# Kernel tuning notes

Measured on AMD Instinct MI355X. Metric: run time of the kernel, lower is better.

## Reference

```python
import jax, jax.numpy as jnp
import numpy as np

MARGIN = 0.3  # init kwarg, mode='norm'


def _pairwise_dist(X):
    # squared euclidean distances, then safe sqrt (matches euc_dist(X.t()).sqrt())
    sq = jnp.sum(X * X, axis=1)                      # [n]
    d2 = sq[:, None] + sq[None, :] - 2.0 * (X @ X.T)  # [n, n]
    d2 = jnp.maximum(d2, 0.0)
    # safe sqrt: avoid inf derivative at 0 (diagonal); forward value identical
    return jnp.where(d2 > 0.0, jnp.sqrt(jnp.where(d2 > 0.0, d2, 1.0)), 0.0)


def setup_inputs() -> dict:
    key = jax.random.key(0)
    kx, ky = jax.random.split(key)
    X = jax.random.normal(kx, (4096, 2048), dtype=jnp.float32)
    Y = jax.random.randint(ky, (4096,), 0, 128, dtype=jnp.int64)
    return {"X": X, "Y": Y}


def reference(X, Y):
    dist = _pairwise_dist(X)                         # [n, n]
    mask = Y[:, None] == Y[None, :]                  # same-identity mask [n, n]
    inf = jnp.array(jnp.inf, dtype=dist.dtype)
    # hardest positive per anchor: max over same-label entries
    dist_ap = jnp.max(jnp.where(mask, dist, -inf), axis=1)  # [n]
    # hardest negative per anchor: min over different-label entries
    dist_an = jnp.min(jnp.where(mask, inf, dist), axis=1)   # [n]
    # mode == 'norm': mean hinge
    return jnp.mean(jnp.maximum(dist_ap - dist_an + MARGIN, 0.0))
```

## Files before the change

### kernel.cpp

```cpp
#include <hip/hip_runtime.h>
#include <hip/hip_bf16.h>
#include <hip/hip_fp8.h>

typedef __attribute__((ext_vector_type(4))) int i32x4;
typedef __attribute__((ext_vector_type(8))) int i32x8;
typedef __attribute__((ext_vector_type(16))) float f32x16;

#define MARGIN 0.3f
#define BIGF 3.0e38f

__device__ __forceinline__ f32x16 mx_mfma(i32x8 a, i32x8 b, f32x16 c) {
    return __builtin_amdgcn_mfma_scale_f32_32x32x64_f8f6f4(
        a, b, c, 0 , 0 ,
        0, 127 , 0, 127 );
}

__device__ __forceinline__ i32x8 ld32(const unsigned char* p) {
    i32x4 lo = *(const i32x4*)p;
    i32x4 hi = *(const i32x4*)(p + 16);
    return __builtin_shufflevector(lo, hi, 0, 1, 2, 3, 4, 5, 6, 7);
}

__global__ __launch_bounds__(256) void convert_norm_kernel(
    const float* __restrict__ X, unsigned char* __restrict__ Xf,
    float* __restrict__ nrm, unsigned* __restrict__ ap,
    unsigned* __restrict__ an, unsigned* __restrict__ cnt, int K) {
    const int wave = threadIdx.x >> 6, lane = threadIdx.x & 63;
    const int row = blockIdx.x * 4 + wave;
    const float* xr = X + (size_t)row * K;
    const size_t pbase = ((size_t)(row >> 5)) << 16;
    const int rsub = row & 31;
    float s = 0.0f;
    for (int c = lane * 8; c < K; c += 64 * 8) {
        float4 v0 = *(const float4*)(xr + c);
        float4 v1 = *(const float4*)(xr + c + 4);
        float f[8] = {v0.x, v0.y, v0.z, v0.w, v1.x, v1.y, v1.z, v1.w};
        union { unsigned char b[8]; uint2 u; } p;
#pragma unroll
        for (int i = 0; i < 8; i++) {
            __hip_fp8_e4m3 q(f[i]);
            p.b[i] = q.__x;
            float d = (float)q;
            s += d * d;
        }
        const int lslot = rsub + (((c >> 5) & 1) << 5);
        unsigned char* dst = Xf + pbase + ((size_t)(c >> 6) << 11)
                             + (lslot << 5) + (c & 31);
        *(uint2*)dst = p.u;
    }
    for (int off = 32; off > 0; off >>= 1) s += __shfl_xor(s, off, 64);
    if (lane == 0) {
        nrm[row] = s;
        ap[row] = 0u;
        an[row] = 0x7F800000u;
        if (row == 0) *cnt = 0u;
    }
}

__global__ __launch_bounds__(256, 4) void gemm_reduce_kernel(
    const unsigned char* __restrict__ Xf, const float* __restrict__ nrm,
    const int* __restrict__ Y, unsigned* __restrict__ ap,
    unsigned* __restrict__ an, unsigned* __restrict__ cnt,
    float* __restrict__ out, int N, int K) {
    __shared__ int sYr[128], sYc[128];
    __shared__ float sNr[128], sNc[128];
    __shared__ float redmax[4][64], redmin[4][64];
    __shared__ float cmax[4][64], cmin[4][64];
    __shared__ float lsum[4];
    __shared__ unsigned s_done;

    const int tid = threadIdx.x;
    const int wave = tid >> 6;
    const int lane = tid & 63;
    const int m = lane & 31;
    const int h = lane >> 5;
    const int wr = wave >> 1;
    const int wc = wave & 1;

    const int NB = N >> 7;
    int bi = blockIdx.x, ti = 0;
    while (bi >= NB - ti) { bi -= NB - ti; ti++; }
    const int tj = ti + bi;
    const int rowBase = ti << 7;
    const int colBase = tj << 7;

    if (tid < 128) {
        sYr[tid] = Y[rowBase + tid];
        sNr[tid] = nrm[rowBase + tid];
    } else {
        const int t0 = tid - 128;
        sYc[t0] = Y[colBase + t0];
        sNc[t0] = nrm[colBase + t0];
    }

    f32x16 acc[2][2];
#pragma unroll
    for (int si = 0; si < 2; si++)
#pragma unroll
        for (int sj = 0; sj < 2; sj++)
#pragma unroll
            for (int rr = 0; rr < 16; rr++) acc[si][sj][rr] = 0.0f;

    const unsigned char* pa[2];
    const unsigned char* pb[2];
#pragma unroll
    for (int si = 0; si < 2; si++)
        pa[si] = Xf + (((size_t)(rowBase >> 5) + wr * 2 + si) << 16) + lane * 32;
#pragma unroll
    for (int sj = 0; sj < 2; sj++)
        pb[sj] = Xf + (((size_t)(colBase >> 5) + wc * 2 + sj) << 16) + lane * 32;

    const int nt = K >> 6;
#pragma unroll 4
    for (int t = 0; t < nt; t++) {
        const size_t off = (size_t)t << 11;
        i32x8 a0 = ld32(pa[0] + off);
        i32x8 a1 = ld32(pa[1] + off);
        i32x8 b0 = ld32(pb[0] + off);
        i32x8 b1 = ld32(pb[1] + off);
        acc[0][0] = mx_mfma(a0, b0, acc[0][0]);
        acc[0][1] = mx_mfma(a0, b1, acc[0][1]);
        acc[1][0] = mx_mfma(a1, b0, acc[1][0]);
        acc[1][1] = mx_mfma(a1, b1, acc[1][1]);
    }

    __syncthreads();

    float cdp[2] = {-1.0f, -1.0f};
    float cdn[2] = {BIGF, BIGF};
#pragma unroll
    for (int si = 0; si < 2; si++)
#pragma unroll
        for (int reg = 0; reg < 16; reg++) {
            const int row64 = si * 32 + (reg & 3) + 8 * (reg >> 2) + 4 * h;
            const int rIdx = wr * 64 + row64;
            const int yr = sYr[rIdx];
            const float nr = sNr[rIdx];
            float dp = -1.0f, dn = BIGF;
#pragma unroll
            for (int sj = 0; sj < 2; sj++) {
                const int cIdx = wc * 64 + sj * 32 + m;
                float d2 = nr + sNc[cIdx] - 2.0f * acc[si][sj][reg];
                float d = sqrtf(fmaxf(d2, 0.0f));
                bool same = (yr == sYc[cIdx]);
                float vp = same ? d : -1.0f;
                float vn = same ? BIGF : d;
                dp = fmaxf(dp, vp);
                dn = fminf(dn, vn);
                cdp[sj] = fmaxf(cdp[sj], vp);
                cdn[sj] = fminf(cdn[sj], vn);
            }
            for (int off = 1; off < 32; off <<= 1) {
                dp = fmaxf(dp, __shfl_xor(dp, off, 64));
                dn = fminf(dn, __shfl_xor(dn, off, 64));
            }
            if (m == 0) {
                redmax[wave][row64] = dp;
                redmin[wave][row64] = dn;
            }
        }
#pragma unroll
    for (int sj = 0; sj < 2; sj++) {
        cdp[sj] = fmaxf(cdp[sj], __shfl_xor(cdp[sj], 32, 64));
        cdn[sj] = fminf(cdn[sj], __shfl_xor(cdn[sj], 32, 64));
        if (h == 0) {
            cmax[wave][sj * 32 + m] = cdp[sj];
            cmin[wave][sj * 32 + m] = cdn[sj];
        }
    }
    __syncthreads();

    if (tid < 128) {
        const int wr2 = tid >> 6, r64 = tid & 63;
        float mx = fmaxf(redmax[wr2 * 2][r64], redmax[wr2 * 2 + 1][r64]);
        float mn = fminf(redmin[wr2 * 2][r64], redmin[wr2 * 2 + 1][r64]);
        atomicMax(&ap[rowBase + tid], __float_as_uint(fmaxf(mx, 0.0f)));
        atomicMin(&an[rowBase + tid], __float_as_uint(mn));
    } else {
        const int t0 = tid - 128;
        const int wc2 = t0 >> 6, c64 = t0 & 63;
        float mx = fmaxf(cmax[wc2][c64], cmax[2 + wc2][c64]);
        float mn = fminf(cmin[wc2][c64], cmin[2 + wc2][c64]);
        atomicMax(&ap[colBase + t0], __float_as_uint(fmaxf(mx, 0.0f)));
        atomicMin(&an[colBase + t0], __float_as_uint(mn));
    }

    __syncthreads();
    if (tid == 0) {
        __threadfence();
        s_done = atomicAdd(cnt, 1u);
    }
    __syncthreads();
    if (s_done == gridDim.x - 1) {
        __threadfence();
        float s = 0.0f;
        for (int i = tid; i < N; i += 256) {
            unsigned ua = __hip_atomic_load(&ap[i], __ATOMIC_RELAXED,
                                            __HIP_MEMORY_SCOPE_AGENT);
            unsigned ub = __hip_atomic_load(&an[i], __ATOMIC_RELAXED,
                                            __HIP_MEMORY_SCOPE_AGENT);
            s += fmaxf(__uint_as_float(ua) - __uint_as_float(ub) + MARGIN, 0.0f);
        }
        for (int off = 32; off > 0; off >>= 1) s += __shfl_xor(s, off, 64);
        if (lane == 0) lsum[wave] = s;
        __syncthreads();
        if (tid == 0)
            out[0] = (lsum[0] + lsum[1] + lsum[2] + lsum[3]) / (float)N;
    }
}

extern "C" void kernel_launch(void* const* d_in, const int* in_sizes, int n_in,
                              void* d_out, int out_size, void* d_ws, size_t ws_size,
                              hipStream_t stream) {
    const float* X = (const float*)d_in[0];
    const int* Y = (const int*)d_in[1];
    float* out = (float*)d_out;
    const int N = in_sizes[1];
    const int K = in_sizes[0] / N;

    char* ws = (char*)d_ws;
    unsigned char* Xf = (unsigned char*)ws;
    float* nrm = (float*)(ws + (size_t)N * K);
    unsigned* ap = (unsigned*)((char*)nrm + (size_t)N * 4);
    unsigned* an = (unsigned*)((char*)ap + (size_t)N * 4);
    unsigned* cnt = (unsigned*)((char*)an + (size_t)N * 4);

    convert_norm_kernel<<<N / 4, 256, 0, stream>>>(X, Xf, nrm, ap, an, cnt, K);
    const int NB = N / 128;
    const int ntri = NB * (NB + 1) / 2;
    gemm_reduce_kernel<<<ntri, 256, 0, stream>>>(Xf, nrm, Y, ap, an, cnt,
                                                 out, N, K);
}
```

Before: 133.4 us.

## Split last 16 triangular tiles into 64x64 quarter blocks to balance tail

The final 16 upper-triangle 128x128 tiles are each split into four 64x64 sub-tiles handled by separate blocks, giving 64 smaller blocks in place of 16 large ones. Each wave in these blocks computes a single 32x32 MFMA tile and pushes row and column reductions straight to global atomics. The aim is to shorten the tail wave of the grid (528 blocks over the CU count) and spread the last work more evenly. The cost is more global atomics and re-reading A/B panels across the quarter blocks.

```diff
diff --git a/kernel.cpp b/kernel.cpp
--- a/kernel.cpp
+++ b/kernel.cpp
@@ -78,111 +78,175 @@
     const int wc = wave & 1;
 
     const int NB = N >> 7;
-    int bi = blockIdx.x, ti = 0;
-    while (bi >= NB - ti) { bi -= NB - ti; ti++; }
-    const int tj = ti + bi;
-    const int rowBase = ti << 7;
-    const int colBase = tj << 7;
-
-    if (tid < 128) {
-        sYr[tid] = Y[rowBase + tid];
-        sNr[tid] = nrm[rowBase + tid];
+    const int ntri = NB * (NB + 1) / 2;
+    const int FULLB = ntri - 16;
+    const int nt = K >> 6;
+
+    if ((int)blockIdx.x < FULLB) {
+        int bi = blockIdx.x, ti = 0;
+        while (bi >= NB - ti) { bi -= NB - ti; ti++; }
+        const int tj = ti + bi;
+        const int rowBase = ti << 7;
+        const int colBase = tj << 7;
+
+        if (tid < 128) {
+            sYr[tid] = Y[rowBase + tid];
+            sNr[tid] = nrm[rowBase + tid];
+        } else {
+            const int t0 = tid - 128;
+            sYc[t0] = Y[colBase + t0];
+            sNc[t0] = nrm[colBase + t0];
+        }
+
+        f32x16 acc[2][2];
+#pragma unroll
+        for (int si = 0; si < 2; si++)
+#pragma unroll
+            for (int sj = 0; sj < 2; sj++)
+#pragma unroll
+                for (int rr = 0; rr < 16; rr++) acc[si][sj][rr] = 0.0f;
+
+        const unsigned char* pa[2];
+        const unsigned char* pb[2];
+#pragma unroll
+        for (int si = 0; si < 2; si++)
+            pa[si] = Xf + (((size_t)(rowBase >> 5) + wr * 2 + si) << 16) + lane * 32;
+#pragma unroll
+        for (int sj = 0; sj < 2; sj++)
+            pb[sj] = Xf + (((size_t)(colBase >> 5) + wc * 2 + sj) << 16) + lane * 32;
+
+#pragma unroll 4
+        for (int t = 0; t < nt; t++) {
+            const size_t off = (size_t)t << 11;
+            i32x8 a0 = ld32(pa[0] + off);
+            i32x8 a1 = ld32(pa[1] + off);
+            i32x8 b0 = ld32(pb[0] + off);
+            i32x8 b1 = ld32(pb[1] + off);
+            acc[0][0] = mx_mfma(a0, b0, acc[0][0]);
+            acc[0][1] = mx_mfma(a0, b1, acc[0][1]);
+            acc[1][0] = mx_mfma(a1, b0, acc[1][0]);
+            acc[1][1] = mx_mfma(a1, b1, acc[1][1]);
+        }
+
+        __syncthreads();
+
+        float cdp[2] = {-1.0f, -1.0f};
+        float cdn[2] = {BIGF, BIGF};
+#pragma unroll
+        for (int si = 0; si < 2; si++)
+#pragma unroll
+            for (int reg = 0; reg < 16; reg++) {
+                const int row64 = si * 32 + (reg & 3) + 8 * (reg >> 2) + 4 * h;
+                const int rIdx = wr * 64 + row64;
+                const int yr = sYr[rIdx];
+                const float nr = sNr[rIdx];
+                float dp = -1.0f, dn = BIGF;
+#pragma unroll
+                for (int sj = 0; sj < 2; sj++) {
+                    const int cIdx = wc * 64 + sj * 32 + m;
+                    float d2 = nr + sNc[cIdx] - 2.0f * acc[si][sj][reg];
+                    float d = sqrtf(fmaxf(d2, 0.0f));
+                    bool same = (yr == sYc[cIdx]);
+                    float vp = same ? d : -1.0f;
+                    float vn = same ? BIGF : d;
+                    dp = fmaxf(dp, vp);
+                    dn = fminf(dn, vn);
+                    cdp[sj] = fmaxf(cdp[sj], vp);
+                    cdn[sj] = fminf(cdn[sj], vn);
+                }
+                for (int off = 1; off < 32; off <<= 1) {
+                    dp = fmaxf(dp, __shfl_xor(dp, off, 64));
+                    dn = fminf(dn, __shfl_xor(dn, off, 64));
+                }
+                if (m == 0) {
+                    redmax[wave][row64] = dp;
+                    redmin[wave][row64] = dn;
+                }
+            }
+#pragma unroll
+        for (int sj = 0; sj < 2; sj++) {
+            cdp[sj] = fmaxf(cdp[sj], __shfl_xor(cdp[sj], 32, 64));
+            cdn[sj] = fminf(cdn[sj], __shfl_xor(cdn[sj], 32, 64));
+            if (h == 0) {
+                cmax[wave][sj * 32 + m] = cdp[sj];
+                cmin[wave][sj * 32 + m] = cdn[sj];
+            }
+        }
+        __syncthreads();
+
+        if (tid < 128) {
+            const int wr2 = tid >> 6, r64 = tid & 63;
+            float mx = fmaxf(redmax[wr2 * 2][r64], redmax[wr2 * 2 + 1][r64]);
+            float mn = fminf(redmin[wr2 * 2][r64], redmin[wr2 * 2 + 1][r64]);
+            atomicMax(&ap[rowBase + tid], __float_as_uint(fmaxf(mx, 0.0f)));
+            atomicMin(&an[rowBase + tid], __float_as_uint(mn));
+        } else {
+            const int t0 = tid - 128;
+            const int wc2 = t0 >> 6, c64 = t0 & 63;
+            float mx = fmaxf(cmax[wc2][c64], cmax[2 + wc2][c64]);
+            float mn = fminf(cmin[wc2][c64], cmin[2 + wc2][c64]);
+            atomicMax(&ap[colBase + t0], __float_as_uint(fmaxf(mx, 0.0f)));
+            atomicMin(&an[colBase + t0], __float_as_uint(mn));
+        }
     } else {
-        const int t0 = tid - 128;
-        sYc[t0] = Y[colBase + t0];
-        sNc[t0] = nrm[colBase + t0];
-    }
-
-    f32x16 acc[2][2];
-#pragma unroll
-    for (int si = 0; si < 2; si++)
-#pragma unroll
-        for (int sj = 0; sj < 2; sj++)
-#pragma unroll
-            for (int rr = 0; rr < 16; rr++) acc[si][sj][rr] = 0.0f;
-
-    const unsigned char* pa[2];
-    const unsigned char* pb[2];
-#pragma unroll
-    for (int si = 0; si < 2; si++)
-        pa[si] = Xf + (((size_t)(rowBase >> 5) + wr * 2 + si) << 16) + lane * 32;
-#pragma unroll
-    for (int sj = 0; sj < 2; sj++)
-        pb[sj] = Xf + (((size_t)(colBase >> 5) + wc * 2 + sj) << 16) + lane * 32;
-
-    const int nt = K >> 6;
+        const int qid = blockIdx.x - FULLB;
+        int bi = FULLB + (qid >> 2), ti = 0;
+        while (bi >= NB - ti) { bi -= NB - ti; ti++; }
+        const int tj = ti + bi;
+        const int q = qid & 3;
+        const int rowBase = (ti << 7) + ((q >> 1) << 6);
+        const int colBase = (tj << 7) + ((q & 1) << 6);
+
+        f32x16 acc;
+#pragma unroll
+        for (int rr = 0; rr < 16; rr++) acc[rr] = 0.0f;
+
+        const unsigned char* pa =
+            Xf + (((size_t)(rowBase >> 5) + wr) << 16) + lane * 32;
+        const unsigned char* pb =
+            Xf + (((size_t)(colBase >> 5) + wc) << 16) + lane * 32;
+
 #pragma unroll 4
-    for (int t = 0; t < nt; t++) {
-        const size_t off = (size_t)t << 11;
-        i32x8 a0 = ld32(pa[0] + off);
-        i32x8 a1 = ld32(pa[1] + off);
-        i32x8 b0 = ld32(pb[0] + off);
-        i32x8 b1 = ld32(pb[1] + off);
-        acc[0][0] = mx_mfma(a0, b0, acc[0][0]);
-        acc[0][1] = mx_mfma(a0, b1, acc[0][1]);
-        acc[1][0] = mx_mfma(a1, b0, acc[1][0]);
-        acc[1][1] = mx_mfma(a1, b1, acc[1][1]);
-    }
-
-    __syncthreads();
-
-    float cdp[2] = {-1.0f, -1.0f};
-    float cdn[2] = {BIGF, BIGF};
-#pragma unroll
-    for (int si = 0; si < 2; si++)
+        for (int t = 0; t < nt; t++) {
+            const size_t off = (size_t)t << 11;
+            i32x8 a = ld32(pa + off);
+            i32x8 b = ld32(pb + off);
+            acc = mx_mfma(a, b, acc);
+        }
+
+        const int gc = colBase + wc * 32 + m;
+        const int yc = Y[gc];
+        const float nc = nrm[gc];
+        float cdp = -1.0f, cdn = BIGF;
 #pragma unroll
         for (int reg = 0; reg < 16; reg++) {
-            const int row64 = si * 32 + (reg & 3) + 8 * (reg >> 2) + 4 * h;
-            const int rIdx = wr * 64 + row64;
-            const int yr = sYr[rIdx];
-            const float nr = sNr[rIdx];
-            float dp = -1.0f, dn = BIGF;
-#pragma unroll
-            for (int sj = 0; sj < 2; sj++) {
-                const int cIdx = wc * 64 + sj * 32 + m;
-                float d2 = nr + sNc[cIdx] - 2.0f * acc[si][sj][reg];
-                float d = sqrtf(fmaxf(d2, 0.0f));
-                bool same = (yr == sYc[cIdx]);
-                float vp = same ? d : -1.0f;
-                float vn = same ? BIGF : d;
-                dp = fmaxf(dp, vp);
-                dn = fminf(dn, vn);
-                cdp[sj] = fmaxf(cdp[sj], vp);
-                cdn[sj] = fminf(cdn[sj], vn);
-            }
+            const int row32 = (reg & 3) + 8 * (reg >> 2) + 4 * h;
+            const int gr = rowBase + wr * 32 + row32;
+            const int yr = Y[gr];
+            const float nr = nrm[gr];
+            float d2 = nr + nc - 2.0f * acc[reg];
+            float d = sqrtf(fmaxf(d2, 0.0f));
+            bool same = (yr == yc);
+            float vp = same ? d : -1.0f;
+            float vn = same ? BIGF : d;
+            cdp = fmaxf(cdp, vp);
+            cdn = fminf(cdn, vn);
+            float dp = vp, dn = vn;
             for (int off = 1; off < 32; off <<= 1) {
                 dp = fmaxf(dp, __shfl_xor(dp, off, 64));
                 dn = fminf(dn, __shfl_xor(dn, off, 64));
             }
             if (m == 0) {
-                redmax[wave][row64] = dp;
-                redmin[wave][row64] = dn;
-            }
-        }
-#pragma unroll
-    for (int sj = 0; sj < 2; sj++) {
-        cdp[sj] = fmaxf(cdp[sj], __shfl_xor(cdp[sj], 32, 64));
-        cdn[sj] = fminf(cdn[sj], __shfl_xor(cdn[sj], 32, 64));
+                atomicMax(&ap[gr], __float_as_uint(fmaxf(dp, 0.0f)));
+                atomicMin(&an[gr], __float_as_uint(dn));
+            }
+        }
+        cdp = fmaxf(cdp, __shfl_xor(cdp, 32, 64));
+        cdn = fminf(cdn, __shfl_xor(cdn, 32, 64));
         if (h == 0) {
-            cmax[wave][sj * 32 + m] = cdp[sj];
-            cmin[wave][sj * 32 + m] = cdn[sj];
-        }
-    }
-    __syncthreads();
-
-    if (tid < 128) {
-        const int wr2 = tid >> 6, r64 = tid & 63;
-        float mx = fmaxf(redmax[wr2 * 2][r64], redmax[wr2 * 2 + 1][r64]);
-        float mn = fminf(redmin[wr2 * 2][r64], redmin[wr2 * 2 + 1][r64]);
-        atomicMax(&ap[rowBase + tid], __float_as_uint(fmaxf(mx, 0.0f)));
-        atomicMin(&an[rowBase + tid], __float_as_uint(mn));
-    } else {
-        const int t0 = tid - 128;
-        const int wc2 = t0 >> 6, c64 = t0 & 63;
-        float mx = fmaxf(cmax[wc2][c64], cmax[2 + wc2][c64]);
-        float mn = fminf(cmin[wc2][c64], cmin[2 + wc2][c64]);
-        atomicMax(&ap[colBase + t0], __float_as_uint(fmaxf(mx, 0.0f)));
-        atomicMin(&an[colBase + t0], __float_as_uint(mn));
+            atomicMax(&ap[gc], __float_as_uint(fmaxf(cdp, 0.0f)));
+            atomicMin(&an[gc], __float_as_uint(cdn));
+        }
     }
 
     __syncthreads();
@@ -228,6 +292,7 @@
     convert_norm_kernel<<<N / 4, 256, 0, stream>>>(X, Xf, nrm, ap, an, cnt, K);
     const int NB = N / 128;
     const int ntri = NB * (NB + 1) / 2;
-    gemm_reduce_kernel<<<ntri, 256, 0, stream>>>(Xf, nrm, Y, ap, an, cnt,
+    const int grid = (ntri - 16) + 64;
+    gemm_reduce_kernel<<<grid, 256, 0, stream>>>(Xf, nrm, Y, ap, an, cnt,
                                                  out, N, K);
 }
```

After: 132.2 us. About the same (-0.9%).
